# Kernel optimization log

Hardware: AMD Instinct MI355X
Metric: run time of the kernel (lower is better)

The kernel has to match this reference:

```python
import jax, jax.numpy as jnp
import numpy as np

B, TE, TD, E, H, V, A, MAXOOV = 8, 400, 100, 128, 256, 50000, 612, 50
VEXT = V + MAXOOV


def setup_inputs():
    key = jax.random.key(0)
    it = iter(jax.random.split(key, 40))
    def nrm(shape, s=0.05):
        return jax.random.normal(next(it), shape, jnp.float32) * s
    inp = {
        "encoder_tokens": jax.random.randint(next(it), (B, TE), 0, V, dtype=jnp.int32),
        "decoder_tokens": jax.random.randint(next(it), (B, TD), 0, V, dtype=jnp.int32),
        "encoder_ext_tokens": jax.random.randint(next(it), (B, TE), 0, VEXT, dtype=jnp.int32),
        "encoder_mask": jnp.ones((B, TE), jnp.float32),
        "embedding": nrm((V, E)),
        "Wih_f": nrm((E, 4 * H)), "Whh_f": nrm((H, 4 * H)), "b_f": jnp.zeros((4 * H,), jnp.float32),
        "Wih_b": nrm((E, 4 * H)), "Whh_b": nrm((H, 4 * H)), "b_b": jnp.zeros((4 * H,), jnp.float32),
        "Wred": nrm((2 * H, H)), "bred": jnp.zeros((H,), jnp.float32),
        "Wenc_feat": nrm((2 * H, A)), "benc_feat": jnp.zeros((A,), jnp.float32),
        "v": nrm((A,), 1.0),
        "Wx": nrm((E + 2 * H, E)), "bx": jnp.zeros((E,), jnp.float32),
        "Wih_d": nrm((E, 4 * H)), "Whh_d": nrm((H, 4 * H)), "b_d": jnp.zeros((4 * H,), jnp.float32),
        "Wdf": nrm((TD, 2 * H, A)), "bdf": jnp.zeros((TD, A), jnp.float32),
        "Wpg": nrm((2 * H + H + H + E, 1)), "bpg": jnp.zeros((1,), jnp.float32),
        "Wout": nrm((H + 2 * H, H)), "bout": jnp.zeros((H,), jnp.float32),
        "Wv": nrm((H, V)), "bv": jnp.zeros((V,), jnp.float32),
    }
    return inp


def _lstm(xs, Wih, Whh, b):
    # xs: [T, B, E] -> outputs [T, B, H], final (h, c)
    def step(carry, x):
        h, c = carry
        g = x @ Wih + h @ Whh + b
        i, f, gg, o = jnp.split(g, 4, axis=-1)  # torch gate order i,f,g,o
        c = jax.nn.sigmoid(f) * c + jax.nn.sigmoid(i) * jnp.tanh(gg)
        h = jax.nn.sigmoid(o) * jnp.tanh(c)
        return (h, c), h
    z = jnp.zeros((xs.shape[1], Whh.shape[0]), xs.dtype)
    (hT, cT), hs = jax.lax.scan(step, (z, z), xs)
    return hs, hT, cT


def reference(encoder_tokens, decoder_tokens, encoder_ext_tokens, encoder_mask,
              embedding, Wih_f, Whh_f, b_f, Wih_b, Whh_b, b_b, Wred, bred,
              Wenc_feat, benc_feat, v, Wx, bx, Wih_d, Whh_d, b_d, Wdf, bdf,
              Wpg, bpg, Wout, bout, Wv, bv):
    # ---- bidirectional LSTM encoder (full-length sequences, mask == 1) ----
    enc_emb = embedding[encoder_tokens]               # [B, TE, E]
    xs = enc_emb.transpose(1, 0, 2)                   # [TE, B, E]
    hf, hTf, cTf = _lstm(xs, Wih_f, Whh_f, b_f)
    hb_rev, hTb, cTb = _lstm(xs[::-1], Wih_b, Whh_b, b_b)
    hb = hb_rev[::-1]
    enc_out = jnp.concatenate([hf, hb], -1).transpose(1, 0, 2)  # [B, TE, 2H]

    # ---- state reducer (original uses reduce_h_layer for BOTH h and c) ----
    h0 = jax.nn.relu(jnp.concatenate([hTf, hTb], -1) @ Wred + bred)
    c0 = jax.nn.relu(jnp.concatenate([cTf, cTb], -1) @ Wred + bred)

    # ---- 1x1 conv == linear on encoder states ----
    enc_feat = enc_out @ Wenc_feat + benc_feat        # [B, TE, A]

    dec_emb = embedding[decoder_tokens].transpose(1, 0, 2)  # [TD, B, E]

    def dec_step(carry, xs_t):
        h, c, ctx = carry
        emb_t, Wdf_t, bdf_t = xs_t
        x = jnp.concatenate([emb_t, ctx], -1) @ Wx + bx          # [B, E]
        g = x @ Wih_d + h @ Whh_d + b_d
        i, f, gg, o = jnp.split(g, 4, axis=-1)
        c = jax.nn.sigmoid(f) * c + jax.nn.sigmoid(i) * jnp.tanh(gg)
        h = jax.nn.sigmoid(o) * jnp.tanh(c)
        dec_feat = jnp.concatenate([h, c], -1) @ Wdf_t + bdf_t   # [B, A] (per-step weights)
        e = jnp.einsum('a,bta->bt', v, jnp.tanh(enc_feat + dec_feat[:, None, :]))
        attn = jax.nn.softmax(e, axis=-1) * encoder_mask
        attn = attn / attn.sum(-1, keepdims=True)
        ctx = jnp.einsum('bt,btd->bd', attn, enc_out)            # [B, 2H]
        p_gen = jax.nn.sigmoid(jnp.concatenate([ctx, h, c, x], -1) @ Wpg + bpg)  # [B, 1]
        out = jnp.concatenate([h, ctx], -1) @ Wout + bout        # [B, H]
        return (h, c, ctx), (out, attn, p_gen)

    ctx0 = jnp.zeros((enc_out.shape[0], 2 * H), enc_out.dtype)
    _, (outs, attns, pgens) = jax.lax.scan(dec_step, (h0, c0, ctx0), (dec_emb, Wdf, bdf))
    # outs [TD,B,H], attns [TD,B,TE], pgens [TD,B,1]

    # ---- pointer-generator mixture over extended vocab ----
    vocab_dist = jax.nn.softmax(outs @ Wv + bv, axis=-1)         # [TD, B, V]
    vocab_dist = pgens * vocab_dist
    attn_w = (1.0 - pgens) * attns                               # [TD, B, TE]

    def scatter_one(a, idx):
        return jnp.zeros((VEXT,), a.dtype).at[idx].add(a)
    copy_dist = jax.vmap(jax.vmap(scatter_one, in_axes=(0, 0)), in_axes=(0, None))(
        attn_w, encoder_ext_tokens)                              # [TD, B, VEXT]

    extra = jnp.zeros(vocab_dist.shape[:2] + (MAXOOV,), vocab_dist.dtype)
    final = jnp.concatenate([vocab_dist, extra], -1) + copy_dist # [TD, B, VEXT]
    return final
```

## Files before the change

kernel.cpp:

```cpp
#include <hip/hip_runtime.h>

#define DEVI __device__ __forceinline__

constexpr int B_ = 8, TE_ = 400, TD_ = 100, E_ = 128, H_ = 256;
constexpr int A_ = 612, V_ = 50000, VEXT_ = 50050;
constexpr int H4_ = 1024, H2_ = 512;
constexpr int NS_ = 16, SLW_ = 40;

constexpr size_t OFS_HBF  = 0;
constexpr size_t OFS_HBB  = 4096;
constexpr size_t OFS_CT   = 8192;
constexpr size_t OFS_CHC  = 12288;
constexpr size_t OFS_PG   = 32896;
constexpr size_t OFS_SROW = 33696;
constexpr size_t OFS_FLG  = 34496;
constexpr size_t OFS_ATT  = 35520;
constexpr size_t OFS_EO   = 355520;
constexpr size_t OFS_OUTS = OFS_EO;
constexpr size_t OFS_EF   = OFS_EO + (size_t)B_*TE_*H2_;

constexpr size_t DO_GINF = 0;
constexpr size_t DO_GINB = DO_GINF + (size_t)TE_*B_*H4_;
constexpr size_t DO_GDEC = 2ull*(size_t)TE_*B_*H4_;
constexpr size_t DO_XPRE = DO_GDEC + (size_t)TD_*B_*H4_;
constexpr size_t DO_CTXH = DO_XPRE + (size_t)TD_*B_*E_;
constexpr size_t DO_HCH  = DO_CTXH + (size_t)TD_*B_*H2_;
constexpr size_t DO_WCG  = DO_HCH + (size_t)TD_*B_*H2_;
constexpr size_t DO_EOWT = DO_WCG + (size_t)H2_*H4_;
constexpr size_t DO_EPB  = DO_EOWT + (size_t)B_*H4_*TE_;

#if defined(__has_builtin)
#if __has_builtin(__builtin_amdgcn_rcpf)
#define HAS_RCPF 1
#endif
#endif

DEVI float rcp_fast(float x) {
#ifdef HAS_RCPF
  return __builtin_amdgcn_rcpf(x);
#else
  return 1.0f / x;
#endif
}

DEVI float sigm(float x) { return rcp_fast(1.0f + __expf(-x)); }
DEVI float tanh_fast(float x) {
  float e = __expf(2.0f * x);
  return 1.0f - 2.0f * rcp_fast(e + 1.0f);
}

DEVI float ld_at(const float* p) {
  unsigned u = __hip_atomic_load((const unsigned*)p, __ATOMIC_RELAXED, __HIP_MEMORY_SCOPE_AGENT);
  return __uint_as_float(u);
}
DEVI void st_at(float* p, float v) {
  __hip_atomic_store((unsigned*)p, __float_as_uint(v), __ATOMIC_RELAXED, __HIP_MEMORY_SCOPE_AGENT);
}

#define WAIT_VM() do { asm volatile("s_waitcnt vmcnt(0)" ::: "memory"); \
                       __builtin_amdgcn_sched_barrier(0); } while (0)

DEVI float wave_max(float v) {
#pragma unroll
  for (int o = 32; o; o >>= 1) v = fmaxf(v, __shfl_xor(v, o));
  return v;
}
DEVI float wave_sum(float v) {
#pragma unroll
  for (int o = 32; o; o >>= 1) v += __shfl_xor(v, o);
  return v;
}

DEVI void flag_bar(unsigned* flags, int ncheck, int slot, unsigned ep, int stride) {
  __syncthreads();
  if (threadIdx.x == 0) {
    asm volatile("s_waitcnt vmcnt(0)" ::: "memory");
    __hip_atomic_store(&flags[slot * stride], ep, __ATOMIC_RELAXED, __HIP_MEMORY_SCOPE_AGENT);
  }
  if ((int)threadIdx.x < ncheck) {
    while (__hip_atomic_load(&flags[threadIdx.x * stride], __ATOMIC_RELAXED,
                             __HIP_MEMORY_SCOPE_AGENT) < ep) {
      __builtin_amdgcn_s_sleep(2);
    }
  }
  __syncthreads();
  asm volatile("" ::: "memory");
}

__global__ __launch_bounds__(256) void k0_wcg(
    const float* __restrict__ Wx, const float* __restrict__ Wih_d,
    float* __restrict__ dob, float* __restrict__ ws)
{
  __shared__ float AsT[32 * 64];
  __shared__ float Bsh[32 * 64];
  const float* Am = Wx + 128 * 128;
  float* C = dob + DO_WCG;
  const int ct = blockIdx.x, rt = blockIdx.y, tid = threadIdx.x;
  if (ct == 0 && rt == 0) {
    for (int i = tid; i < 8192; i += 256) ws[OFS_HBF + i] = 0.0f;
    unsigned* f = (unsigned*)(ws + OFS_FLG);
    for (int i = tid; i < 1024; i += 256) f[i] = 0u;
  }
  const int c0 = ct * 64, r0 = rt * 64;
  const int tx = tid & 15, ty = tid >> 4;
  float4 acc0 = make_float4(0,0,0,0), acc1 = acc0, acc2 = acc0, acc3 = acc0;
  for (int kc = 0; kc < 4; ++kc) {
#pragma unroll
    for (int i = 0; i < 2; ++i) {
      int q = tid * 2 + i;
      int r = q >> 3, kq = q & 7;
      float4 v = *(const float4*)&Am[(size_t)(r0 + r) * 128 + kc * 32 + kq * 4];
      AsT[(kq * 4 + 0) * 64 + r] = v.x; AsT[(kq * 4 + 1) * 64 + r] = v.y;
      AsT[(kq * 4 + 2) * 64 + r] = v.z; AsT[(kq * 4 + 3) * 64 + r] = v.w;
    }
#pragma unroll
    for (int i = 0; i < 2; ++i) {
      int q = tid * 2 + i;
      int kk = q >> 4, cq = q & 15;
      *(float4*)&Bsh[kk * 64 + cq * 4] =
          *(const float4*)&Wih_d[(size_t)(kc * 32 + kk) * H4_ + c0 + cq * 4];
    }
    __syncthreads();
#pragma unroll
    for (int kk = 0; kk < 32; ++kk) {
      float4 w4 = *(float4*)&Bsh[kk * 64 + tx * 4];
      const float* ar = &AsT[kk * 64 + ty * 4];
      acc0.x += ar[0]*w4.x; acc0.y += ar[0]*w4.y; acc0.z += ar[0]*w4.z; acc0.w += ar[0]*w4.w;
      acc1.x += ar[1]*w4.x; acc1.y += ar[1]*w4.y; acc1.z += ar[1]*w4.z; acc1.w += ar[1]*w4.w;
      acc2.x += ar[2]*w4.x; acc2.y += ar[2]*w4.y; acc2.z += ar[2]*w4.z; acc2.w += ar[2]*w4.w;
      acc3.x += ar[3]*w4.x; acc3.y += ar[3]*w4.y; acc3.z += ar[3]*w4.z; acc3.w += ar[3]*w4.w;
    }
    __syncthreads();
  }
  float4 r4[4] = {acc0, acc1, acc2, acc3};
#pragma unroll
  for (int i = 0; i < 4; ++i)
    *(float4*)&C[(size_t)(r0 + ty * 4 + i) * H4_ + c0 + tx * 4] = r4[i];
}

__global__ __launch_bounds__(256) void k1_embed_gates(
    const int* __restrict__ etok, const float* __restrict__ emb,
    const float* __restrict__ Wih_f, const float* __restrict__ b_f,
    const float* __restrict__ Wih_b, const float* __restrict__ b_b,
    float* __restrict__ gin_f, float* __restrict__ gin_b)
{
  __shared__ float er[8 * 128];
  const int t = blockIdx.x, tid = threadIdx.x;
  for (int i = tid; i < 1024; i += 256) {
    int b = i >> 7, e = i & 127;
    er[i] = emb[(size_t)etok[b * TE_ + t] * E_ + e];
  }
  __syncthreads();
  float bfv[4], bbv[4];
#pragma unroll
  for (int g = 0; g < 4; ++g) { bfv[g] = b_f[g * H_ + tid]; bbv[g] = b_b[g * H_ + tid]; }
  float af[32], ab[32];
#pragma unroll
  for (int i = 0; i < 32; ++i) { af[i] = bfv[i & 3]; ab[i] = bbv[i & 3]; }
  for (int e = 0; e < E_; ++e) {
    float wf[4], wb[4];
#pragma unroll
    for (int g = 0; g < 4; ++g) {
      wf[g] = Wih_f[(size_t)e * H4_ + g * H_ + tid];
      wb[g] = Wih_b[(size_t)e * H4_ + g * H_ + tid];
    }
#pragma unroll
    for (int b = 0; b < 8; ++b) {
      float x = er[b * 128 + e];
#pragma unroll
      for (int g = 0; g < 4; ++g) { af[b * 4 + g] += x * wf[g]; ab[b * 4 + g] += x * wb[g]; }
    }
  }
#pragma unroll
  for (int b = 0; b < 8; ++b)
#pragma unroll
    for (int g = 0; g < 4; ++g) {
      gin_f[((size_t)t * 8 + b) * H4_ + g * H_ + tid] = af[b * 4 + g];
      gin_b[((size_t)t * 8 + b) * H4_ + g * H_ + tid] = ab[b * 4 + g];
    }
}

__global__ __launch_bounds__(256) void k1d_dec_pre(
    const int* __restrict__ dtok, const float* __restrict__ emb,
    const float* __restrict__ Wx, const float* __restrict__ bx,
    const float* __restrict__ Wih_d, const float* __restrict__ b_d,
    float* __restrict__ dob)
{
  __shared__ float er[8 * 128];
  __shared__ float xl[8 * 128];
  const int t = blockIdx.x, tid = threadIdx.x;
  for (int i = tid; i < 1024; i += 256) {
    int b = i >> 7, e = i & 127;
    er[i] = emb[(size_t)dtok[b * TD_ + t] * E_ + e];
  }
  __syncthreads();
  {
    const int col = tid & 127, bh = tid >> 7;
#pragma unroll
    for (int ii = 0; ii < 4; ++ii) {
      int b = bh + (ii << 1);
      float acc = bx[col];
      for (int k = 0; k < 128; ++k) acc += er[b * 128 + k] * Wx[(size_t)k * E_ + col];
      xl[b * 128 + col] = acc;
      dob[DO_XPRE + ((size_t)t * 8 + b) * E_ + col] = acc;
    }
  }
  __syncthreads();
  float bv[4];
#pragma unroll
  for (int g = 0; g < 4; ++g) bv[g] = b_d[g * H_ + tid];
  float af[32];
#pragma unroll
  for (int i = 0; i < 32; ++i) af[i] = bv[i & 3];
  for (int e = 0; e < E_; ++e) {
    float w[4];
#pragma unroll
    for (int g = 0; g < 4; ++g) w[g] = Wih_d[(size_t)e * H4_ + g * H_ + tid];
#pragma unroll
    for (int b = 0; b < 8; ++b) {
      float x = xl[b * 128 + e];
#pragma unroll
      for (int g = 0; g < 4; ++g) af[b * 4 + g] += x * w[g];
    }
  }
#pragma unroll
  for (int b = 0; b < 8; ++b)
#pragma unroll
    for (int g = 0; g < 4; ++g)
      dob[DO_GDEC + ((size_t)t * 8 + b) * H4_ + g * H_ + tid] = af[b * 4 + g];
}

__global__ __launch_bounds__(256, 1) void k2_encoder_scan(
    const float* __restrict__ gin_f, const float* __restrict__ gin_b,
    const float* __restrict__ Whh_f, const float* __restrict__ Whh_b,
    float* __restrict__ ws)
{
  __shared__ float sm[4096];
  const int bid = blockIdx.x, tid = threadIdx.x;
  const int dir = bid >> 5, c0 = (bid & 31) * 8;
  const float* Whh = dir ? Whh_b : Whh_f;
  const float* gin = dir ? gin_b : gin_f;
  float* hb = ws + (dir ? OFS_HBB : OFS_HBF);
  float* cT = ws + OFS_CT;
  float* eo = ws + OFS_EO;
  unsigned* flg = (unsigned*)(ws + OFS_FLG) + (dir ? 128 : 0);
  const int slot = bid & 31;

  const int jl = tid >> 3, kg = tid & 7;
  const int gt = jl >> 3, hcl = jl & 7;
  const int jcol = gt * H_ + c0 + hcl;
  float wreg[32];
#pragma unroll
  for (int kk = 0; kk < 32; ++kk) wreg[kk] = Whh[(size_t)(kg + kk * 8) * H4_ + jcol];

  const int uhc = tid >> 3, ub = tid & 7;
  float c_reg = 0.0f;
  unsigned ep = 0;

  for (int t = 0; t < TE_; ++t) {
    const int te = dir ? (TE_ - 1 - t) : t;
    float* hrd = hb + (t & 1) * 2048;
    float* hwr = hb + ((t & 1) ^ 1) * 2048;
    float gpre[4] = {0, 0, 0, 0};
    if (tid < 64) {
#pragma unroll
      for (int gg = 0; gg < 4; ++gg)
        gpre[gg] = gin[((size_t)te * 8 + ub) * H4_ + gg * H_ + c0 + uhc];
    }
    {
      float4 v0, v1;
      const float* a0 = &hrd[tid * 8];
      const float* a1 = &hrd[tid * 8 + 4];
      asm volatile(
          "global_load_dwordx4 %0, %2, off sc0 sc1\n\t"
          "global_load_dwordx4 %1, %3, off sc0 sc1"
          : "=&v"(v0), "=&v"(v1) : "v"(a0), "v"(a1));
      WAIT_VM();
      *(float4*)&sm[tid * 8] = v0;
      *(float4*)&sm[tid * 8 + 4] = v1;
    }
    __syncthreads();
    float acc[8] = {0, 0, 0, 0, 0, 0, 0, 0};
#pragma unroll
    for (int kk = 0; kk < 32; ++kk) {
      float w = wreg[kk];
      const float* hp = &sm[(kg + kk * 8) * 8];
#pragma unroll
      for (int b = 0; b < 8; ++b) acc[b] += hp[b] * w;
    }
    float* part = sm + 2048;
    *(float4*)&part[(jl * 8 + kg) * 8]     = make_float4(acc[0], acc[1], acc[2], acc[3]);
    *(float4*)&part[(jl * 8 + kg) * 8 + 4] = make_float4(acc[4], acc[5], acc[6], acc[7]);
    __syncthreads();
    if (tid < 64) {
      float g[4];
#pragma unroll
      for (int gg = 0; gg < 4; ++gg) {
        float s = gpre[gg];
#pragma unroll
        for (int k2 = 0; k2 < 8; ++k2) s += part[((gg * 8 + uhc) * 8 + k2) * 8 + ub];
        g[gg] = s;
      }
      float ci = sigm(g[0]), cf = sigm(g[1]), cg = tanh_fast(g[2]), co = sigm(g[3]);
      c_reg = cf * c_reg + ci * cg;
      float hn = co * tanh_fast(c_reg);
      st_at(&hwr[(c0 + uhc) * 8 + ub], hn);
      eo[((size_t)ub * TE_ + te) * H2_ + dir * H_ + c0 + uhc] = hn;
      if (t == TE_ - 1) cT[ub * H2_ + dir * H_ + c0 + uhc] = c_reg;
    }
    ep++; flag_bar(flg, 32, slot, ep, 4);
  }
}

__global__ __launch_bounds__(256) void k3_encfeat(
    const float* __restrict__ eo, const float* __restrict__ Wef,
    const float* __restrict__ bef, float* __restrict__ ef)
{
  __shared__ float AsT[32 * 64];
  __shared__ float Wsh[32 * 64];
  const int ct = blockIdx.x, rt = blockIdx.y, tid = threadIdx.x;
  const int c0 = ct * 64, r0 = rt * 64;
  const int tx = tid & 15, ty = tid >> 4;
  float4 acc0 = make_float4(0,0,0,0), acc1 = acc0, acc2 = acc0, acc3 = acc0;
  for (int kc = 0; kc < 16; ++kc) {
#pragma unroll
    for (int i = 0; i < 2; ++i) {
      int q = tid * 2 + i;
      int r = q >> 3, kq = q & 7;
      float4 v = *(const float4*)&eo[(size_t)(r0 + r) * H2_ + kc * 32 + kq * 4];
      AsT[(kq * 4 + 0) * 64 + r] = v.x; AsT[(kq * 4 + 1) * 64 + r] = v.y;
      AsT[(kq * 4 + 2) * 64 + r] = v.z; AsT[(kq * 4 + 3) * 64 + r] = v.w;
    }
#pragma unroll
    for (int i = 0; i < 2; ++i) {
      int q = tid * 2 + i;
      int kk = q >> 4, cq = q & 15;
      int col = c0 + cq * 4;
      float4 v = make_float4(0,0,0,0);
      if (col < A_) v = *(const float4*)&Wef[(size_t)(kc * 32 + kk) * A_ + col];
      *(float4*)&Wsh[kk * 64 + cq * 4] = v;
    }
    __syncthreads();
#pragma unroll
    for (int kk = 0; kk < 32; ++kk) {
      float4 w4 = *(float4*)&Wsh[kk * 64 + tx * 4];
      const float* ar = &AsT[kk * 64 + ty * 4];
      acc0.x += ar[0]*w4.x; acc0.y += ar[0]*w4.y; acc0.z += ar[0]*w4.z; acc0.w += ar[0]*w4.w;
      acc1.x += ar[1]*w4.x; acc1.y += ar[1]*w4.y; acc1.z += ar[1]*w4.z; acc1.w += ar[1]*w4.w;
      acc2.x += ar[2]*w4.x; acc2.y += ar[2]*w4.y; acc2.z += ar[2]*w4.z; acc2.w += ar[2]*w4.w;
      acc3.x += ar[3]*w4.x; acc3.y += ar[3]*w4.y; acc3.z += ar[3]*w4.z; acc3.w += ar[3]*w4.w;
    }
    __syncthreads();
  }
  const int col = c0 + tx * 4;
  if (col < A_) {
    float4 bb = *(const float4*)&bef[col];
    float4 r4[4] = {acc0, acc1, acc2, acc3};
#pragma unroll
    for (int i = 0; i < 4; ++i) {
      int row = r0 + ty * 4 + i;
      float4 o = make_float4(r4[i].x + bb.x, r4[i].y + bb.y, r4[i].z + bb.z, r4[i].w + bb.w);
      *(float4*)&ef[(size_t)row * A_ + col] = o;
    }
  }
}

__global__ __launch_bounds__(256) void k3b_eowt(
    const float* __restrict__ eo, const float* __restrict__ dob_c, float* __restrict__ dob)
{
  __shared__ float Wt[32 * 64];
  __shared__ float Et[32 * 40];
  const float* Wcg = dob_c + DO_WCG;
  float* eoWT = dob + DO_EOWT;
  const int jt = blockIdx.x, tt = blockIdx.y, b = blockIdx.z, tid = threadIdx.x;
  const int j0 = jt * 64, te0 = tt * 40;
  const int j_l = tid & 63, tq = tid >> 6;
  float acc[10];
#pragma unroll
  for (int u = 0; u < 10; ++u) acc[u] = 0.0f;
  for (int kc = 0; kc < 16; ++kc) {
#pragma unroll
    for (int i = 0; i < 2; ++i) {
      int q = tid * 2 + i;
      int kk = q >> 4, j4 = q & 15;
      *(float4*)&Wt[kk * 64 + j4 * 4] =
          *(const float4*)&Wcg[(size_t)(kc * 32 + kk) * H4_ + j0 + j4 * 4];
    }
#pragma unroll
    for (int i = 0; i < 2; ++i) {
      int q = tid + i * 256;
      if (q < 320) {
        int te_l = q >> 3, kq = q & 7;
        float4 v = *(const float4*)&eo[((size_t)b * TE_ + te0 + te_l) * H2_ + kc * 32 + kq * 4];
// ... 253 lines not shown
      __syncthreads();

      if (tid < TE_) {
        const float* efp = &efG[((size_t)b * TE_ + tid) * A_ + a0];
        float acc = 0.0f;
        for (int q = 0; q < nq; ++q) {
          float4 e4 = *(const float4*)&efp[q * 4];
          const float* dd = &dfl[q * 4];
          const float* vv = &vvL[q * 4];
          acc += vv[0] * tanh_fast(e4.x + dd[0]);
          acc += vv[1] * tanh_fast(e4.y + dd[1]);
          acc += vv[2] * tanh_fast(e4.z + dd[2]);
          acc += vv[3] * tanh_fast(e4.w + dd[3]);
        }
        st_at(&epb[((size_t)b * TE_ + tid) * 16 + s], acc);
      }
      asm volatile("" :: "v"(dm));
    }
    epg++; flag_bar(flgG, 16, s, epg, 4);
  }
}

__global__ __launch_bounds__(256) void k4c_ctx(
    const float* __restrict__ ws, float* __restrict__ dob)
{
  __shared__ float AsT[32 * 64];
  __shared__ float Bsh[32 * 64];
  const float* att = ws + OFS_ATT;
  const float* eo  = ws + OFS_EO;
  float* ctxh = dob + DO_CTXH;
  const int ct = blockIdx.x, rt = blockIdx.y, b = blockIdx.z, tid = threadIdx.x;
  const int c0 = ct * 64, r0 = rt * 64;
  const int tx = tid & 15, ty = tid >> 4;
  float4 acc0 = make_float4(0,0,0,0), acc1 = acc0, acc2 = acc0, acc3 = acc0;
  for (int kc = 0; kc < 13; ++kc) {
#pragma unroll
    for (int i = 0; i < 2; ++i) {
      int q = tid * 2 + i;
      int r = q >> 3, kq = q & 7;
      int k = kc * 32 + kq * 4;
      float4 v = make_float4(0, 0, 0, 0);
      if (k < TE_ && r0 + r < TD_)
        v = *(const float4*)&att[((size_t)(r0 + r) * 8 + b) * TE_ + k];
      AsT[(kq * 4 + 0) * 64 + r] = v.x; AsT[(kq * 4 + 1) * 64 + r] = v.y;
      AsT[(kq * 4 + 2) * 64 + r] = v.z; AsT[(kq * 4 + 3) * 64 + r] = v.w;
    }
#pragma unroll
    for (int i = 0; i < 2; ++i) {
      int q = tid * 2 + i;
      int kk = q >> 4, cq = q & 15;
      int k = kc * 32 + kk;
      float4 v = make_float4(0, 0, 0, 0);
      if (k < TE_) v = *(const float4*)&eo[((size_t)b * TE_ + k) * H2_ + c0 + cq * 4];
      *(float4*)&Bsh[kk * 64 + cq * 4] = v;
    }
    __syncthreads();
#pragma unroll
    for (int kk = 0; kk < 32; ++kk) {
      float4 w4 = *(float4*)&Bsh[kk * 64 + tx * 4];
      const float* ar = &AsT[kk * 64 + ty * 4];
      acc0.x += ar[0]*w4.x; acc0.y += ar[0]*w4.y; acc0.z += ar[0]*w4.z; acc0.w += ar[0]*w4.w;
      acc1.x += ar[1]*w4.x; acc1.y += ar[1]*w4.y; acc1.z += ar[1]*w4.z; acc1.w += ar[1]*w4.w;
      acc2.x += ar[2]*w4.x; acc2.y += ar[2]*w4.y; acc2.z += ar[2]*w4.z; acc2.w += ar[2]*w4.w;
      acc3.x += ar[3]*w4.x; acc3.y += ar[3]*w4.y; acc3.z += ar[3]*w4.z; acc3.w += ar[3]*w4.w;
    }
    __syncthreads();
  }
  float4 r4[4] = {acc0, acc1, acc2, acc3};
#pragma unroll
  for (int i = 0; i < 4; ++i) {
    int row = r0 + ty * 4 + i;
    if (row < TD_)
      *(float4*)&ctxh[((size_t)row * 8 + b) * H2_ + c0 + tx * 4] = r4[i];
  }
}

__global__ __launch_bounds__(256) void k4b_post(
    const float* __restrict__ Wx, const float* __restrict__ Wout, const float* __restrict__ bout,
    const float* __restrict__ Wpg, const float* __restrict__ bpg,
    float* __restrict__ ws, const float* __restrict__ dob)
{
  __shared__ float hcl[4096], ctxl[4096], cpl[4096], xl[1024], red2[256];
  const int t = blockIdx.x, tid = threadIdx.x;
  const float* hch  = dob + DO_HCH;
  const float* ctxh = dob + DO_CTXH;
  const float* xpre = dob + DO_XPRE;
  for (int i = tid; i < 4096; i += 256) {
    hcl[i]  = hch[(size_t)t * 4096 + i];
    ctxl[i] = ctxh[(size_t)t * 4096 + i];
    cpl[i]  = t ? ctxh[(size_t)(t - 1) * 4096 + i] : 0.0f;
  }
  __syncthreads();
  {
    const int col = tid & 127, bh = tid >> 7;
#pragma unroll
    for (int ii = 0; ii < 4; ++ii) {
      int b = bh + (ii << 1);
      float acc = xpre[(size_t)t * 1024 + b * E_ + col];
      for (int k = 0; k < H2_; ++k) acc += cpl[b * H2_ + k] * Wx[(size_t)(128 + k) * E_ + col];
      xl[b * E_ + col] = acc;
    }
  }
  __syncthreads();
  {
    const int col = tid;
    for (int b = 0; b < 8; ++b) {
      float acc = bout[col];
      for (int k = 0; k < 768; ++k)
        acc += (k < H_ ? hcl[b * H2_ + k] : ctxl[b * H2_ + (k - H_)]) * Wout[(size_t)k * H_ + col];
      ws[OFS_OUTS + ((size_t)t * 8 + b) * H_ + col] = acc;
    }
  }
  {
    const int b = tid >> 5, sg = tid & 31;
    float acc = 0.0f;
    for (int j = 0; j < 36; ++j) {
      int k = sg * 36 + j;
      float xv;
      if (k < H2_)       xv = ctxl[b * H2_ + k];
      else if (k < 768)  xv = hcl[b * H2_ + (k - H2_)];
      else if (k < 1024) xv = hcl[b * H2_ + H_ + (k - 768)];
      else               xv = xl[b * E_ + (k - 1024)];
      acc += xv * Wpg[k];
    }
    red2[tid] = acc;
    __syncthreads();
    if (tid < 8) {
      float s = 0.0f;
      for (int k2 = 0; k2 < 32; ++k2) s += red2[tid * 32 + k2];
      ws[OFS_PG + t * 8 + tid] = sigm(s + bpg[0]);
    }
  }
}

__global__ __launch_bounds__(256) void k5a_logits(
    const float* __restrict__ outs, const float* __restrict__ Wv,
    const float* __restrict__ bv, float* __restrict__ out)
{
  __shared__ float aT[32 * 64];
  __shared__ float wl[32 * 256];
  const int rt = blockIdx.x, ct = blockIdx.y, tid = threadIdx.x;
  const int r0 = rt * 64, c0 = ct * 256;
  const int cq = tid & 63, rg = tid >> 6;
  float4 acc[16];
#pragma unroll
  for (int i = 0; i < 16; ++i) acc[i] = make_float4(0, 0, 0, 0);
  for (int kc = 0; kc < 8; ++kc) {
#pragma unroll
    for (int i = 0; i < 2; ++i) {
      int q = tid * 2 + i;
      int r = q >> 3, kq = q & 7;
      float4 v = make_float4(0, 0, 0, 0);
      if (r0 + r < 800) v = *(const float4*)&outs[(size_t)(r0 + r) * H_ + kc * 32 + kq * 4];
      aT[(kq * 4 + 0) * 64 + r] = v.x; aT[(kq * 4 + 1) * 64 + r] = v.y;
      aT[(kq * 4 + 2) * 64 + r] = v.z; aT[(kq * 4 + 3) * 64 + r] = v.w;
    }
#pragma unroll
    for (int i = 0; i < 8; ++i) {
      int q = tid + i * 256;
      int kk = q >> 6, c4 = q & 63;
      int col = c0 + c4 * 4;
      float4 v = make_float4(0, 0, 0, 0);
      if (col < V_) v = *(const float4*)&Wv[(size_t)(kc * 32 + kk) * V_ + col];
      *(float4*)&wl[kk * 256 + c4 * 4] = v;
    }
    __syncthreads();
#pragma unroll
    for (int kk = 0; kk < 32; ++kk) {
      float4 w4 = *(float4*)&wl[kk * 256 + cq * 4];
      const float* ar = &aT[kk * 64 + rg * 16];
#pragma unroll
      for (int rr = 0; rr < 16; ++rr) {
        float a = ar[rr];
        acc[rr].x += a * w4.x; acc[rr].y += a * w4.y;
        acc[rr].z += a * w4.z; acc[rr].w += a * w4.w;
      }
    }
    __syncthreads();
  }
  const int col = c0 + cq * 4;
  if (col < V_) {
    float4 bb = *(const float4*)&bv[col];
#pragma unroll
    for (int rr = 0; rr < 16; ++rr) {
      int row = r0 + rg * 16 + rr;
      if (row < 800) {
        float2 lo = make_float2(acc[rr].x + bb.x, acc[rr].y + bb.y);
        float2 hi = make_float2(acc[rr].z + bb.z, acc[rr].w + bb.w);
        *(float2*)&out[(size_t)row * VEXT_ + col] = lo;
        *(float2*)&out[(size_t)row * VEXT_ + col + 2] = hi;
      }
    }
  }
}

__global__ __launch_bounds__(256) void k5b_rowsum(const float* __restrict__ out, float* __restrict__ Srow)
{
  __shared__ float red[256];
  const int r = blockIdx.x, tid = threadIdx.x;
  const float* base = out + (size_t)r * VEXT_;
  float s = 0.0f;
  for (int i = tid; i < V_ / 2; i += 256) {
    float2 v = *(const float2*)&base[i * 2];
    s += __expf(v.x) + __expf(v.y);
  }
  red[tid] = s; __syncthreads();
  for (int st = 128; st > 0; st >>= 1) { if (tid < st) red[tid] += red[tid + st]; __syncthreads(); }
  if (tid == 0) Srow[r] = red[0];
}

__global__ __launch_bounds__(256) void k5c_final(
    float* __restrict__ out, const float* __restrict__ Srow, const float* __restrict__ pg)
{
  const int cc = blockIdx.x, r = blockIdx.y, tid = threadIdx.x;
  const float scale = pg[r] * rcp_fast(Srow[r]);
  float* base = out + (size_t)r * VEXT_;
#pragma unroll
  for (int i = 0; i < 4; ++i) {
    int col = cc * 2048 + i * 512 + tid * 2;
    if (col < V_) {
      float2 v = *(float2*)&base[col];
      v.x = __expf(v.x) * scale; v.y = __expf(v.y) * scale;
      *(float2*)&base[col] = v;
    } else if (col < VEXT_) {
      *(float2*)&base[col] = make_float2(0.0f, 0.0f);
    }
  }
}

__global__ __launch_bounds__(256) void k5d_scatter(
    float* __restrict__ out, const float* __restrict__ ws, const int* __restrict__ ext)
{
  const int r = blockIdx.x, tid = threadIdx.x;
  const int b = r & 7;
  const float* at = ws + OFS_ATT + (size_t)r * TE_;
  const float w = 1.0f - ws[OFS_PG + r];
  float* base = out + (size_t)r * VEXT_;
  for (int i = tid; i < TE_; i += 256)
    atomicAdd(&base[ext[b * TE_ + i]], w * at[i]);
}

extern "C" void kernel_launch(void* const* d_in, const int* in_sizes, int n_in,
                              void* d_out, int out_size, void* d_ws, size_t ws_size,
                              hipStream_t stream) {
  const int*   etok  = (const int*)d_in[0];
  const int*   dtok  = (const int*)d_in[1];
  const int*   ext   = (const int*)d_in[2];
  const float* maskp = (const float*)d_in[3];
  const float* emb   = (const float*)d_in[4];
  const float* Wih_f = (const float*)d_in[5];
  const float* Whh_f = (const float*)d_in[6];
  const float* b_f   = (const float*)d_in[7];
  const float* Wih_b = (const float*)d_in[8];
  const float* Whh_b = (const float*)d_in[9];
  const float* b_b   = (const float*)d_in[10];
  const float* Wred  = (const float*)d_in[11];
  const float* bred  = (const float*)d_in[12];
  const float* Wef   = (const float*)d_in[13];
  const float* bef   = (const float*)d_in[14];
  const float* vvec  = (const float*)d_in[15];
  const float* Wx    = (const float*)d_in[16];
  const float* bx    = (const float*)d_in[17];
  const float* Wih_d = (const float*)d_in[18];
  const float* Whh_d = (const float*)d_in[19];
  const float* b_d   = (const float*)d_in[20];
  const float* Wdf   = (const float*)d_in[21];
  const float* bdf   = (const float*)d_in[22];
  const float* Wpg   = (const float*)d_in[23];
  const float* bpg   = (const float*)d_in[24];
  const float* Wout  = (const float*)d_in[25];
  const float* bout  = (const float*)d_in[26];
  const float* Wv    = (const float*)d_in[27];
  const float* bv    = (const float*)d_in[28];
  float* out = (float*)d_out;
  float* wsf = (float*)d_ws;
  float* dob = out;

  float* gin_f = dob + DO_GINF;
  float* gin_b = dob + DO_GINB;

  k0_wcg<<<dim3(16, 8), 256, 0, stream>>>(Wx, Wih_d, dob, wsf);
  k1_embed_gates<<<400, 256, 0, stream>>>(etok, emb, Wih_f, b_f, Wih_b, b_b, gin_f, gin_b);
  k1d_dec_pre<<<100, 256, 0, stream>>>(dtok, emb, Wx, bx, Wih_d, b_d, dob);

  {
    void* args2[5] = {(void*)&gin_f, (void*)&gin_b, (void*)&Whh_f, (void*)&Whh_b, (void*)&wsf};
    if (hipLaunchCooperativeKernel((void*)k2_encoder_scan, dim3(64), dim3(256), args2, 0, stream) != hipSuccess)
      k2_encoder_scan<<<64, 256, 0, stream>>>(gin_f, gin_b, Whh_f, Whh_b, wsf);
  }

  k3_encfeat<<<dim3(10, 50), 256, 0, stream>>>(wsf + OFS_EO, Wef, bef, wsf + OFS_EF);
  k3b_eowt<<<dim3(16, 10, 8), 256, 0, stream>>>(wsf + OFS_EO, dob, dob);

  {
    void* args4[9] = {(void*)&maskp, (void*)&Wred, (void*)&bred, (void*)&Whh_d,
                      (void*)&Wdf, (void*)&bdf, (void*)&vvec, (void*)&wsf, (void*)&dob};
    if (hipLaunchCooperativeKernel((void*)k4_decoder, dim3(128), dim3(512), args4, 0, stream) != hipSuccess)
      k4_decoder<<<128, 512, 0, stream>>>(maskp, Wred, bred, Whh_d, Wdf, bdf, vvec, wsf, dob);
  }

  k4c_ctx<<<dim3(8, 2, 8), 256, 0, stream>>>(wsf, dob);
  k4b_post<<<100, 256, 0, stream>>>(Wx, Wout, bout, Wpg, bpg, wsf, dob);

  k5a_logits<<<dim3(13, 196), 256, 0, stream>>>(wsf + OFS_OUTS, Wv, bv, out);
  k5b_rowsum<<<800, 256, 0, stream>>>(out, wsf + OFS_SROW);
  k5c_final<<<dim3(25, 800), 256, 0, stream>>>(out, wsf + OFS_SROW, wsf + OFS_PG);
  k5d_scatter<<<800, 256, 0, stream>>>(out, wsf, ext);
}
```

Before: 3.555 ms.

## Overlap encoder scan with precompute via tagged gates; fuse softmax rowsum into logits

The weight-combine, encoder input-gate and decoder precompute kernels are merged into one cooperative launch alongside the encoder LSTM scan. The scan blocks poll per-element 64-bit gate values whose high word carries a timestep tag, so the scan can start before all input gates exist. Gate blocks are issued in the order the two scan directions consume them. The separate zero-init pass is dropped, with flag waits changed to equality checks. The softmax row-sum kernel is removed; the logits kernel now computes exp partial sums and accumulates them with atomics, which avoids a full re-read of the logits. This relies on stale tags or flags never matching, adds spin-wait traffic, and gives up the deterministic summation order.

```diff
diff --git a/kernel.cpp b/kernel.cpp
--- a/kernel.cpp
+++ b/kernel.cpp
@@ -1,6 +1,7 @@
 #include <hip/hip_runtime.h>
 
 #define DEVI __device__ __forceinline__
+typedef unsigned long long u64;
 
 constexpr int B_ = 8, TE_ = 400, TD_ = 100, E_ = 128, H_ = 256;
 constexpr int A_ = 612, V_ = 50000, VEXT_ = 50050;
@@ -19,9 +20,8 @@
 constexpr size_t OFS_OUTS = OFS_EO;
 constexpr size_t OFS_EF   = OFS_EO + (size_t)B_*TE_*H2_;
 
-constexpr size_t DO_GINF = 0;
-constexpr size_t DO_GINB = DO_GINF + (size_t)TE_*B_*H4_;
-constexpr size_t DO_GDEC = 2ull*(size_t)TE_*B_*H4_;
+constexpr size_t DO_GIN  = 0;
+constexpr size_t DO_GDEC = DO_GIN + 4ull*(size_t)TE_*B_*H4_;
 constexpr size_t DO_XPRE = DO_GDEC + (size_t)TD_*B_*H4_;
 constexpr size_t DO_CTXH = DO_XPRE + (size_t)TD_*B_*E_;
 constexpr size_t DO_HCH  = DO_CTXH + (size_t)TD_*B_*H2_;
@@ -56,6 +56,17 @@
 DEVI void st_at(float* p, float v) {
   __hip_atomic_store((unsigned*)p, __float_as_uint(v), __ATOMIC_RELAXED, __HIP_MEMORY_SCOPE_AGENT);
 }
+DEVI u64 ld64_at(const u64* p) {
+  return __hip_atomic_load(p, __ATOMIC_RELAXED, __HIP_MEMORY_SCOPE_AGENT);
+}
+DEVI void st64_at(u64* p, u64 v) {
+  __hip_atomic_store(p, v, __ATOMIC_RELAXED, __HIP_MEMORY_SCOPE_AGENT);
+}
+DEVI u64 packft(float f, unsigned tag) {
+  return (u64)__float_as_uint(f) | ((u64)tag << 32);
+}
+DEVI float lowf(u64 v) { return __uint_as_float((unsigned)v); }
+DEVI unsigned hitag(u64 v) { return (unsigned)(v >> 32); }
 
 #define WAIT_VM() do { asm volatile("s_waitcnt vmcnt(0)" ::: "memory"); \
                        __builtin_amdgcn_sched_barrier(0); } while (0)
@@ -79,7 +90,7 @@
   }
   if ((int)threadIdx.x < ncheck) {
     while (__hip_atomic_load(&flags[threadIdx.x * stride], __ATOMIC_RELAXED,
-                             __HIP_MEMORY_SCOPE_AGENT) < ep) {
+                             __HIP_MEMORY_SCOPE_AGENT) != ep) {
       __builtin_amdgcn_s_sleep(2);
     }
   }
@@ -87,228 +98,234 @@
   asm volatile("" ::: "memory");
 }
 
-__global__ __launch_bounds__(256) void k0_wcg(
-    const float* __restrict__ Wx, const float* __restrict__ Wih_d,
-    float* __restrict__ dob, float* __restrict__ ws)
-{
-  __shared__ float AsT[32 * 64];
-  __shared__ float Bsh[32 * 64];
-  const float* Am = Wx + 128 * 128;
-  float* C = dob + DO_WCG;
-  const int ct = blockIdx.x, rt = blockIdx.y, tid = threadIdx.x;
-  if (ct == 0 && rt == 0) {
-    for (int i = tid; i < 8192; i += 256) ws[OFS_HBF + i] = 0.0f;
-    unsigned* f = (unsigned*)(ws + OFS_FLG);
-    for (int i = tid; i < 1024; i += 256) f[i] = 0u;
-  }
-  const int c0 = ct * 64, r0 = rt * 64;
-  const int tx = tid & 15, ty = tid >> 4;
-  float4 acc0 = make_float4(0,0,0,0), acc1 = acc0, acc2 = acc0, acc3 = acc0;
-  for (int kc = 0; kc < 4; ++kc) {
-#pragma unroll
-    for (int i = 0; i < 2; ++i) {
-      int q = tid * 2 + i;
-      int r = q >> 3, kq = q & 7;
-      float4 v = *(const float4*)&Am[(size_t)(r0 + r) * 128 + kc * 32 + kq * 4];
-      AsT[(kq * 4 + 0) * 64 + r] = v.x; AsT[(kq * 4 + 1) * 64 + r] = v.y;
-      AsT[(kq * 4 + 2) * 64 + r] = v.z; AsT[(kq * 4 + 3) * 64 + r] = v.w;
-    }
-#pragma unroll
-    for (int i = 0; i < 2; ++i) {
-      int q = tid * 2 + i;
-      int kk = q >> 4, cq = q & 15;
-      *(float4*)&Bsh[kk * 64 + cq * 4] =
-          *(const float4*)&Wih_d[(size_t)(kc * 32 + kk) * H4_ + c0 + cq * 4];
-    }
-    __syncthreads();
-#pragma unroll
-    for (int kk = 0; kk < 32; ++kk) {
-      float4 w4 = *(float4*)&Bsh[kk * 64 + tx * 4];
-      const float* ar = &AsT[kk * 64 + ty * 4];
-      acc0.x += ar[0]*w4.x; acc0.y += ar[0]*w4.y; acc0.z += ar[0]*w4.z; acc0.w += ar[0]*w4.w;
-      acc1.x += ar[1]*w4.x; acc1.y += ar[1]*w4.y; acc1.z += ar[1]*w4.z; acc1.w += ar[1]*w4.w;
-      acc2.x += ar[2]*w4.x; acc2.y += ar[2]*w4.y; acc2.z += ar[2]*w4.z; acc2.w += ar[2]*w4.w;
-      acc3.x += ar[3]*w4.x; acc3.y += ar[3]*w4.y; acc3.z += ar[3]*w4.z; acc3.w += ar[3]*w4.w;
-    }
-    __syncthreads();
-  }
-  float4 r4[4] = {acc0, acc1, acc2, acc3};
-#pragma unroll
-  for (int i = 0; i < 4; ++i)
-    *(float4*)&C[(size_t)(r0 + ty * 4 + i) * H4_ + c0 + tx * 4] = r4[i];
-}
-
-__global__ __launch_bounds__(256) void k1_embed_gates(
+__global__ __launch_bounds__(256, 1) void k2_fused(
     const int* __restrict__ etok, const float* __restrict__ emb,
     const float* __restrict__ Wih_f, const float* __restrict__ b_f,
     const float* __restrict__ Wih_b, const float* __restrict__ b_b,
-    float* __restrict__ gin_f, float* __restrict__ gin_b)
+    const float* __restrict__ Whh_f, const float* __restrict__ Whh_b,
+    const int* __restrict__ dtok, const float* __restrict__ Wx,
+    const float* __restrict__ bx, const float* __restrict__ Wih_d,
+    const float* __restrict__ b_d,
+    float* __restrict__ ws, float* __restrict__ dob)
 {
-  __shared__ float er[8 * 128];
-  const int t = blockIdx.x, tid = threadIdx.x;
-  for (int i = tid; i < 1024; i += 256) {
-    int b = i >> 7, e = i & 127;
-    er[i] = emb[(size_t)etok[b * TE_ + t] * E_ + e];
-  }
-  __syncthreads();
-  float bfv[4], bbv[4];
-#pragma unroll
-  for (int g = 0; g < 4; ++g) { bfv[g] = b_f[g * H_ + tid]; bbv[g] = b_b[g * H_ + tid]; }
-  float af[32], ab[32];
-#pragma unroll
-  for (int i = 0; i < 32; ++i) { af[i] = bfv[i & 3]; ab[i] = bbv[i & 3]; }
-  for (int e = 0; e < E_; ++e) {
-    float wf[4], wb[4];
-#pragma unroll
-    for (int g = 0; g < 4; ++g) {
-      wf[g] = Wih_f[(size_t)e * H4_ + g * H_ + tid];
-      wb[g] = Wih_b[(size_t)e * H4_ + g * H_ + tid];
-    }
-#pragma unroll
-    for (int b = 0; b < 8; ++b) {
-      float x = er[b * 128 + e];
-#pragma unroll
-      for (int g = 0; g < 4; ++g) { af[b * 4 + g] += x * wf[g]; ab[b * 4 + g] += x * wb[g]; }
-    }
-  }
-#pragma unroll
-  for (int b = 0; b < 8; ++b)
-#pragma unroll
-    for (int g = 0; g < 4; ++g) {
-      gin_f[((size_t)t * 8 + b) * H4_ + g * H_ + tid] = af[b * 4 + g];
-      gin_b[((size_t)t * 8 + b) * H4_ + g * H_ + tid] = ab[b * 4 + g];
-    }
-}
-
-__global__ __launch_bounds__(256) void k1d_dec_pre(
-    const int* __restrict__ dtok, const float* __restrict__ emb,
-    const float* __restrict__ Wx, const float* __restrict__ bx,
-    const float* __restrict__ Wih_d, const float* __restrict__ b_d,
-    float* __restrict__ dob)
-{
-  __shared__ float er[8 * 128];
-  __shared__ float xl[8 * 128];
-  const int t = blockIdx.x, tid = threadIdx.x;
-  for (int i = tid; i < 1024; i += 256) {
-    int b = i >> 7, e = i & 127;
-    er[i] = emb[(size_t)dtok[b * TD_ + t] * E_ + e];
-  }
-  __syncthreads();
-  {
-    const int col = tid & 127, bh = tid >> 7;
-#pragma unroll
-    for (int ii = 0; ii < 4; ++ii) {
-      int b = bh + (ii << 1);
-      float acc = bx[col];
-      for (int k = 0; k < 128; ++k) acc += er[b * 128 + k] * Wx[(size_t)k * E_ + col];
-      xl[b * 128 + col] = acc;
-      dob[DO_XPRE + ((size_t)t * 8 + b) * E_ + col] = acc;
-    }
-  }
-  __syncthreads();
-  float bv[4];
-#pragma unroll
-  for (int g = 0; g < 4; ++g) bv[g] = b_d[g * H_ + tid];
-  float af[32];
-#pragma unroll
-  for (int i = 0; i < 32; ++i) af[i] = bv[i & 3];
-  for (int e = 0; e < E_; ++e) {
-    float w[4];
-#pragma unroll
-    for (int g = 0; g < 4; ++g) w[g] = Wih_d[(size_t)e * H4_ + g * H_ + tid];
-#pragma unroll
-    for (int b = 0; b < 8; ++b) {
-      float x = xl[b * 128 + e];
-#pragma unroll
-      for (int g = 0; g < 4; ++g) af[b * 4 + g] += x * w[g];
-    }
-  }
-#pragma unroll
-  for (int b = 0; b < 8; ++b)
-#pragma unroll
-    for (int g = 0; g < 4; ++g)
-      dob[DO_GDEC + ((size_t)t * 8 + b) * H4_ + g * H_ + tid] = af[b * 4 + g];
-}
-
-__global__ __launch_bounds__(256, 1) void k2_encoder_scan(
-    const float* __restrict__ gin_f, const float* __restrict__ gin_b,
-    const float* __restrict__ Whh_f, const float* __restrict__ Whh_b,
-    float* __restrict__ ws)
-{
-  __shared__ float sm[4096];
+  __shared__ float smu[4096];
   const int bid = blockIdx.x, tid = threadIdx.x;
-  const int dir = bid >> 5, c0 = (bid & 31) * 8;
-  const float* Whh = dir ? Whh_b : Whh_f;
-  const float* gin = dir ? gin_b : gin_f;
-  float* hb = ws + (dir ? OFS_HBB : OFS_HBF);
-  float* cT = ws + OFS_CT;
-  float* eo = ws + OFS_EO;
-  unsigned* flg = (unsigned*)(ws + OFS_FLG) + (dir ? 128 : 0);
-  const int slot = bid & 31;
-
-  const int jl = tid >> 3, kg = tid & 7;
-  const int gt = jl >> 3, hcl = jl & 7;
-  const int jcol = gt * H_ + c0 + hcl;
-  float wreg[32];
-#pragma unroll
-  for (int kk = 0; kk < 32; ++kk) wreg[kk] = Whh[(size_t)(kg + kk * 8) * H4_ + jcol];
-
-  const int uhc = tid >> 3, ub = tid & 7;
-  float c_reg = 0.0f;
-  unsigned ep = 0;
-
-  for (int t = 0; t < TE_; ++t) {
-    const int te = dir ? (TE_ - 1 - t) : t;
-    float* hrd = hb + (t & 1) * 2048;
-    float* hwr = hb + ((t & 1) ^ 1) * 2048;
-    float gpre[4] = {0, 0, 0, 0};
-    if (tid < 64) {
-#pragma unroll
-      for (int gg = 0; gg < 4; ++gg)
-        gpre[gg] = gin[((size_t)te * 8 + ub) * H4_ + gg * H_ + c0 + uhc];
-    }
+  u64* ging = (u64*)(dob + DO_GIN);
+
+  if (bid < 64) {
+    float* sm = smu;
+    float* part = smu + 2048;
+    const int dir = bid >> 5, c0 = (bid & 31) * 8;
+    const float* Whh = dir ? Whh_b : Whh_f;
+    float* hb = ws + (dir ? OFS_HBB : OFS_HBF);
+    float* cT = ws + OFS_CT;
+    float* eo = ws + OFS_EO;
+    unsigned* flg = (unsigned*)(ws + OFS_FLG) + (dir ? 128 : 0);
+    const int slot = bid & 31;
+
+    const int jl = tid >> 3, kg = tid & 7;
+    const int gt = jl >> 3, hcl = jl & 7;
+    const int jcol = gt * H_ + c0 + hcl;
+    float wreg[32];
+#pragma unroll
+    for (int kk = 0; kk < 32; ++kk) wreg[kk] = Whh[(size_t)(kg + kk * 8) * H4_ + jcol];
+
+    const int uhc = tid >> 3, ub = tid & 7;
+    float c_reg = 0.0f;
+    unsigned ep = 0;
+
+    for (int t = 0; t < TE_; ++t) {
+      const int te = dir ? (TE_ - 1 - t) : t;
+      float* hrd = hb + (t & 1) * 2048;
+      float* hwr = hb + ((t & 1) ^ 1) * 2048;
+      float4 v0, v1;
+      if (t > 0) {
+        const float* a0 = &hrd[tid * 8];
+        const float* a1 = &hrd[tid * 8 + 4];
+        asm volatile(
+            "global_load_dwordx4 %0, %2, off sc0 sc1\n\t"
+            "global_load_dwordx4 %1, %3, off sc0 sc1"
+            : "=&v"(v0), "=&v"(v1) : "v"(a0), "v"(a1));
+      }
+      float gpre[4] = {0, 0, 0, 0};
+      if (tid < 64) {
+        const u64* gp = ging + (((size_t)dir * TE_ + te) * 8 + ub) * H4_ + c0 + uhc;
+        const unsigned want = (unsigned)(te + 1);
+        u64 g0, g1, g2, g3;
+        bool ok;
+        do {
+          g0 = ld64_at(gp); g1 = ld64_at(gp + 256);
+          g2 = ld64_at(gp + 512); g3 = ld64_at(gp + 768);
+          ok = (hitag(g0) == want) & (hitag(g1) == want) &
+               (hitag(g2) == want) & (hitag(g3) == want);
+          if (!ok) __builtin_amdgcn_s_sleep(1);
+        } while (!ok);
+        gpre[0] = lowf(g0); gpre[1] = lowf(g1);
+        gpre[2] = lowf(g2); gpre[3] = lowf(g3);
+      }
+      if (t > 0) {
+        WAIT_VM();
+        *(float4*)&sm[tid * 8] = v0;
+        *(float4*)&sm[tid * 8 + 4] = v1;
+      } else {
+#pragma unroll
+        for (int i = 0; i < 8; ++i) sm[tid * 8 + i] = 0.0f;
+      }
+      __syncthreads();
+      float acc[8] = {0, 0, 0, 0, 0, 0, 0, 0};
+#pragma unroll
+      for (int kk = 0; kk < 32; ++kk) {
+        float w = wreg[kk];
+        const float* hp = &sm[(kg + kk * 8) * 8];
+#pragma unroll
+        for (int b = 0; b < 8; ++b) acc[b] += hp[b] * w;
+      }
+      *(float4*)&part[(jl * 8 + kg) * 8]     = make_float4(acc[0], acc[1], acc[2], acc[3]);
+      *(float4*)&part[(jl * 8 + kg) * 8 + 4] = make_float4(acc[4], acc[5], acc[6], acc[7]);
+      __syncthreads();
+      if (tid < 64) {
+        float g[4];
+#pragma unroll
+        for (int gg = 0; gg < 4; ++gg) {
+          float s = gpre[gg];
+#pragma unroll
+          for (int k2 = 0; k2 < 8; ++k2) s += part[((gg * 8 + uhc) * 8 + k2) * 8 + ub];
+          g[gg] = s;
+        }
+        float ci = sigm(g[0]), cf = sigm(g[1]), cg = tanh_fast(g[2]), co = sigm(g[3]);
+        c_reg = cf * c_reg + ci * cg;
+        float hn = co * tanh_fast(c_reg);
+        st_at(&hwr[(c0 + uhc) * 8 + ub], hn);
+        eo[((size_t)ub * TE_ + te) * H2_ + dir * H_ + c0 + uhc] = hn;
+        if (t == TE_ - 1) cT[ub * H2_ + dir * H_ + c0 + uhc] = c_reg;
+      }
+      ep++; flag_bar(flg, 32, slot, ep, 4);
+    }
+
+  } else if (bid < 464) {
+    float* er = smu;
+    const int p = bid - 64;
+    const int t = (p & 1) ? (TE_ - 1 - (p >> 1)) : (p >> 1);
+    for (int i = tid; i < 1024; i += 256) {
+      int b = i >> 7, e = i & 127;
+      er[i] = emb[(size_t)etok[b * TE_ + t] * E_ + e];
+    }
+    __syncthreads();
+    float bfv[4], bbv[4];
+#pragma unroll
+    for (int g = 0; g < 4; ++g) { bfv[g] = b_f[g * H_ + tid]; bbv[g] = b_b[g * H_ + tid]; }
+    float af[32], ab[32];
+#pragma unroll
+    for (int i = 0; i < 32; ++i) { af[i] = bfv[i & 3]; ab[i] = bbv[i & 3]; }
+    for (int e = 0; e < E_; ++e) {
+      float wf[4], wb[4];
+#pragma unroll
+      for (int g = 0; g < 4; ++g) {
+        wf[g] = Wih_f[(size_t)e * H4_ + g * H_ + tid];
+        wb[g] = Wih_b[(size_t)e * H4_ + g * H_ + tid];
+      }
+#pragma unroll
+      for (int b = 0; b < 8; ++b) {
+        float x = er[b * 128 + e];
+#pragma unroll
+        for (int g = 0; g < 4; ++g) { af[b * 4 + g] += x * wf[g]; ab[b * 4 + g] += x * wb[g]; }
+      }
+    }
+    const unsigned tag = (unsigned)(t + 1);
+#pragma unroll
+    for (int b = 0; b < 8; ++b)
+#pragma unroll
+      for (int g = 0; g < 4; ++g) {
+        st64_at(&ging[((size_t)t * 8 + b) * H4_ + g * H_ + tid], packft(af[b * 4 + g], tag));
+        st64_at(&ging[(((size_t)TE_ + t) * 8 + b) * H4_ + g * H_ + tid], packft(ab[b * 4 + g], tag));
+      }
+
+  } else if (bid < 592) {
+    float* AsT = smu;
+    float* Bsh = smu + 2048;
+    const float* Am = Wx + 128 * 128;
+    float* C = dob + DO_WCG;
+    const int q0 = bid - 464;
+    const int ct = q0 & 15, rt = q0 >> 4;
+    const int c0 = ct * 64, r0 = rt * 64;
+    const int tx = tid & 15, ty = tid >> 4;
+    float4 acc0 = make_float4(0,0,0,0), acc1 = acc0, acc2 = acc0, acc3 = acc0;
+    for (int kc = 0; kc < 4; ++kc) {
+#pragma unroll
+      for (int i = 0; i < 2; ++i) {
+        int q = tid * 2 + i;
+        int r = q >> 3, kq = q & 7;
+        float4 v = *(const float4*)&Am[(size_t)(r0 + r) * 128 + kc * 32 + kq * 4];
+        AsT[(kq * 4 + 0) * 64 + r] = v.x; AsT[(kq * 4 + 1) * 64 + r] = v.y;
+        AsT[(kq * 4 + 2) * 64 + r] = v.z; AsT[(kq * 4 + 3) * 64 + r] = v.w;
+      }
+#pragma unroll
+      for (int i = 0; i < 2; ++i) {
+        int q = tid * 2 + i;
+        int kk = q >> 4, cq = q & 15;
+        *(float4*)&Bsh[kk * 64 + cq * 4] =
+            *(const float4*)&Wih_d[(size_t)(kc * 32 + kk) * H4_ + c0 + cq * 4];
+      }
+      __syncthreads();
+#pragma unroll
+      for (int kk = 0; kk < 32; ++kk) {
+        float4 w4 = *(float4*)&Bsh[kk * 64 + tx * 4];
+        const float* ar = &AsT[kk * 64 + ty * 4];
+        acc0.x += ar[0]*w4.x; acc0.y += ar[0]*w4.y; acc0.z += ar[0]*w4.z; acc0.w += ar[0]*w4.w;
+        acc1.x += ar[1]*w4.x; acc1.y += ar[1]*w4.y; acc1.z += ar[1]*w4.z; acc1.w += ar[1]*w4.w;
+        acc2.x += ar[2]*w4.x; acc2.y += ar[2]*w4.y; acc2.z += ar[2]*w4.z; acc2.w += ar[2]*w4.w;
+        acc3.x += ar[3]*w4.x; acc3.y += ar[3]*w4.y; acc3.z += ar[3]*w4.z; acc3.w += ar[3]*w4.w;
+      }
+      __syncthreads();
+    }
+    float4 r4[4] = {acc0, acc1, acc2, acc3};
+#pragma unroll
+    for (int i = 0; i < 4; ++i)
+      *(float4*)&C[(size_t)(r0 + ty * 4 + i) * H4_ + c0 + tx * 4] = r4[i];
+
+  } else {
+    float* er = smu;
+    float* xl = smu + 1024;
+    const int t = bid - 592;
+    for (int i = tid; i < 1024; i += 256) {
+      int b = i >> 7, e = i & 127;
+      er[i] = emb[(size_t)dtok[b * TD_ + t] * E_ + e];
+    }
+    __syncthreads();
     {
-      float4 v0, v1;
-      const float* a0 = &hrd[tid * 8];
-      const float* a1 = &hrd[tid * 8 + 4];
-      asm volatile(
-          "global_load_dwordx4 %0, %2, off sc0 sc1\n\t"
-          "global_load_dwordx4 %1, %3, off sc0 sc1"
-          : "=&v"(v0), "=&v"(v1) : "v"(a0), "v"(a1));
-      WAIT_VM();
-      *(float4*)&sm[tid * 8] = v0;
-      *(float4*)&sm[tid * 8 + 4] = v1;
-    }
-    __syncthreads();
-    float acc[8] = {0, 0, 0, 0, 0, 0, 0, 0};
-#pragma unroll
-    for (int kk = 0; kk < 32; ++kk) {
-      float w = wreg[kk];
-      const float* hp = &sm[(kg + kk * 8) * 8];
-#pragma unroll
-      for (int b = 0; b < 8; ++b) acc[b] += hp[b] * w;
-    }
-    float* part = sm + 2048;
-    *(float4*)&part[(jl * 8 + kg) * 8]     = make_float4(acc[0], acc[1], acc[2], acc[3]);
-    *(float4*)&part[(jl * 8 + kg) * 8 + 4] = make_float4(acc[4], acc[5], acc[6], acc[7]);
-    __syncthreads();
-    if (tid < 64) {
-      float g[4];
-#pragma unroll
-      for (int gg = 0; gg < 4; ++gg) {
-        float s = gpre[gg];
-#pragma unroll
-        for (int k2 = 0; k2 < 8; ++k2) s += part[((gg * 8 + uhc) * 8 + k2) * 8 + ub];
-        g[gg] = s;
-      }
-      float ci = sigm(g[0]), cf = sigm(g[1]), cg = tanh_fast(g[2]), co = sigm(g[3]);
-      c_reg = cf * c_reg + ci * cg;
-      float hn = co * tanh_fast(c_reg);
-      st_at(&hwr[(c0 + uhc) * 8 + ub], hn);
-      eo[((size_t)ub * TE_ + te) * H2_ + dir * H_ + c0 + uhc] = hn;
-      if (t == TE_ - 1) cT[ub * H2_ + dir * H_ + c0 + uhc] = c_reg;
-    }
-    ep++; flag_bar(flg, 32, slot, ep, 4);
+      const int col = tid & 127, bh = tid >> 7;
+#pragma unroll
+      for (int ii = 0; ii < 4; ++ii) {
+        int b = bh + (ii << 1);
+        float acc = bx[col];
+        for (int k = 0; k < 128; ++k) acc += er[b * 128 + k] * Wx[(size_t)k * E_ + col];
+        xl[b * 128 + col] = acc;
+        dob[DO_XPRE + ((size_t)t * 8 + b) * E_ + col] = acc;
+      }
+    }
+    __syncthreads();
+    float bv[4];
+#pragma unroll
+    for (int g = 0; g < 4; ++g) bv[g] = b_d[g * H_ + tid];
+    float af[32];
+#pragma unroll
+    for (int i = 0; i < 32; ++i) af[i] = bv[i & 3];
+    for (int e = 0; e < E_; ++e) {
+      float w[4];
+#pragma unroll
+      for (int g = 0; g < 4; ++g) w[g] = Wih_d[(size_t)e * H4_ + g * H_ + tid];
+#pragma unroll
+      for (int b = 0; b < 8; ++b) {
+        float x = xl[b * 128 + e];
+#pragma unroll
+        for (int g = 0; g < 4; ++g) af[b * 4 + g] += x * w[g];
+      }
+    }
+#pragma unroll
+    for (int b = 0; b < 8; ++b)
+#pragma unroll
+      for (int g = 0; g < 4; ++g)
+        dob[DO_GDEC + ((size_t)t * 8 + b) * H4_ + g * H_ + tid] = af[b * 4 + g];
   }
 }
 
@@ -728,6 +745,9 @@
 {
   __shared__ float hcl[4096], ctxl[4096], cpl[4096], xl[1024], red2[256];
   const int t = blockIdx.x, tid = threadIdx.x;
+  if (t == 0) {
+    for (int i = tid; i < 800; i += 256) ws[OFS_SROW + i] = 0.0f;
+  }
   const float* hch  = dob + DO_HCH;
   const float* ctxh = dob + DO_CTXH;
   const float* xpre = dob + DO_XPRE;
@@ -781,10 +801,11 @@
 
 __global__ __launch_bounds__(256) void k5a_logits(
     const float* __restrict__ outs, const float* __restrict__ Wv,
-    const float* __restrict__ bv, float* __restrict__ out)
+    const float* __restrict__ bv, float* __restrict__ out, float* __restrict__ Srow)
 {
   __shared__ float aT[32 * 64];
   __shared__ float wl[32 * 256];
+  __shared__ float esum[64 * 64];
   const int rt = blockIdx.x, ct = blockIdx.y, tid = threadIdx.x;
   const int r0 = rt * 64, c0 = ct * 256;
   const int cq = tid & 63, rg = tid >> 6;
@@ -830,29 +851,32 @@
 #pragma unroll
     for (int rr = 0; rr < 16; ++rr) {
       int row = r0 + rg * 16 + rr;
+      float es = 0.0f;
       if (row < 800) {
-        float2 lo = make_float2(acc[rr].x + bb.x, acc[rr].y + bb.y);
-        float2 hi = make_float2(acc[rr].z + bb.z, acc[rr].w + bb.w);
+        float lx = acc[rr].x + bb.x, ly = acc[rr].y + bb.y;
+        float lz = acc[rr].z + bb.z, lw = acc[rr].w + bb.w;
+        float2 lo = make_float2(lx, ly);
+        float2 hi = make_float2(lz, lw);
         *(float2*)&out[(size_t)row * VEXT_ + col] = lo;
         *(float2*)&out[(size_t)row * VEXT_ + col + 2] = hi;
-      }
-    }
-  }
-}
-
-__global__ __launch_bounds__(256) void k5b_rowsum(const float* __restrict__ out, float* __restrict__ Srow)
-{
-  __shared__ float red[256];
-  const int r = blockIdx.x, tid = threadIdx.x;
-  const float* base = out + (size_t)r * VEXT_;
-  float s = 0.0f;
-  for (int i = tid; i < V_ / 2; i += 256) {
-    float2 v = *(const float2*)&base[i * 2];
-    s += __expf(v.x) + __expf(v.y);
-  }
-  red[tid] = s; __syncthreads();
-  for (int st = 128; st > 0; st >>= 1) { if (tid < st) red[tid] += red[tid + st]; __syncthreads(); }
-  if (tid == 0) Srow[r] = red[0];
+        es = __expf(lx) + __expf(ly) + __expf(lz) + __expf(lw);
+      }
+      esum[(rg * 16 + rr) * 64 + cq] = es;
+    }
+  } else {
+#pragma unroll
+    for (int rr = 0; rr < 16; ++rr) esum[(rg * 16 + rr) * 64 + cq] = 0.0f;
+  }
+  __syncthreads();
+  if (tid < 64) {
+    int row = r0 + tid;
+    if (row < 800) {
+      float s = 0.0f;
+#pragma unroll 16
+      for (int q = 0; q < 64; ++q) s += esum[tid * 64 + q];
+      atomicAdd(&Srow[row], s);
+    }
+  }
 }
 
 __global__ __launch_bounds__(256) void k5c_final(
@@ -922,17 +946,14 @@
   float* wsf = (float*)d_ws;
   float* dob = out;
 
-  float* gin_f = dob + DO_GINF;
-  float* gin_b = dob + DO_GINB;
-
-  k0_wcg<<<dim3(16, 8), 256, 0, stream>>>(Wx, Wih_d, dob, wsf);
-  k1_embed_gates<<<400, 256, 0, stream>>>(etok, emb, Wih_f, b_f, Wih_b, b_b, gin_f, gin_b);
-  k1d_dec_pre<<<100, 256, 0, stream>>>(dtok, emb, Wx, bx, Wih_d, b_d, dob);
-
   {
-    void* args2[5] = {(void*)&gin_f, (void*)&gin_b, (void*)&Whh_f, (void*)&Whh_b, (void*)&wsf};
-    if (hipLaunchCooperativeKernel((void*)k2_encoder_scan, dim3(64), dim3(256), args2, 0, stream) != hipSuccess)
-      k2_encoder_scan<<<64, 256, 0, stream>>>(gin_f, gin_b, Whh_f, Whh_b, wsf);
+    void* args2[15] = {(void*)&etok, (void*)&emb, (void*)&Wih_f, (void*)&b_f,
+                       (void*)&Wih_b, (void*)&b_b, (void*)&Whh_f, (void*)&Whh_b,
+                       (void*)&dtok, (void*)&Wx, (void*)&bx, (void*)&Wih_d,
+                       (void*)&b_d, (void*)&wsf, (void*)&dob};
+    if (hipLaunchCooperativeKernel((void*)k2_fused, dim3(692), dim3(256), args2, 0, stream) != hipSuccess)
+      k2_fused<<<692, 256, 0, stream>>>(etok, emb, Wih_f, b_f, Wih_b, b_b, Whh_f, Whh_b,
+                                        dtok, Wx, bx, Wih_d, b_d, wsf, dob);
   }
 
   k3_encfeat<<<dim3(10, 50), 256, 0, stream>>>(wsf + OFS_EO, Wef, bef, wsf + OFS_EF);
@@ -948,8 +969,10 @@
   k4c_ctx<<<dim3(8, 2, 8), 256, 0, stream>>>(wsf, dob);
   k4b_post<<<100, 256, 0, stream>>>(Wx, Wout, bout, Wpg, bpg, wsf, dob);
 
-  k5a_logits<<<dim3(13, 196), 256, 0, stream>>>(wsf + OFS_OUTS, Wv, bv, out);
-  k5b_rowsum<<<800, 256, 0, stream>>>(out, wsf + OFS_SROW);
+  {
+    float* srow = wsf + OFS_SROW;
+    k5a_logits<<<dim3(13, 196), 256, 0, stream>>>(wsf + OFS_OUTS, Wv, bv, out, srow);
+  }
   k5c_final<<<dim3(25, 800), 256, 0, stream>>>(out, wsf + OFS_SROW, wsf + OFS_PG);
   k5d_scatter<<<800, 256, 0, stream>>>(out, wsf, ext);
 }
```

Result: slower. 3.698 ms (+4.0%).
